# Optimization experiments

Measured on AMD Instinct MI355X. Metric: run time of the kernel, lower is better.

Reference implementation:

```python
import jax, jax.numpy as jnp
import numpy as np

NUM_BUOYS = 16384
TIME_STEPS = 8
FEATURE_DIM = 64
ID_EMB_DIM = 1024  # must equal gru_hidden_size for steps 4/5 to type-check
HIDDEN = 1024
NUM_EMB = 100
INPUT_SIZE = FEATURE_DIM + ID_EMB_DIM


def setup_inputs() -> dict:
    key = jax.random.key(0)
    k = jax.random.split(key, 7)
    s = 1.0 / np.sqrt(HIDDEN)
    return {
        "buoy_obs": jax.random.normal(k[0], (NUM_BUOYS, TIME_STEPS, FEATURE_DIM), jnp.float32),
        "buoy_ids": jax.random.randint(k[1], (NUM_BUOYS,), 0, NUM_EMB),
        "emb": jax.random.normal(k[2], (NUM_EMB, ID_EMB_DIM), jnp.float32),
        "W_ih": jax.random.uniform(k[3], (3 * HIDDEN, INPUT_SIZE), jnp.float32, -s, s),
        "W_hh": jax.random.uniform(k[4], (3 * HIDDEN, HIDDEN), jnp.float32, -s, s),
        "b_ih": jax.random.uniform(k[5], (3 * HIDDEN,), jnp.float32, -s, s),
        "b_hh": jax.random.uniform(k[6], (3 * HIDDEN,), jnp.float32, -s, s),
    }


def _gru_cell(x, h, W_ih, W_hh, b_ih, b_hh):
    # PyTorch GRU gate layout: [r, z, n]
    gi = x @ W_ih.T + b_ih  # (N, 3H)
    gh = h @ W_hh.T + b_hh  # (N, 3H)
    gi_r, gi_z, gi_n = jnp.split(gi, 3, axis=-1)
    gh_r, gh_z, gh_n = jnp.split(gh, 3, axis=-1)
    r = jax.nn.sigmoid(gi_r + gh_r)
    z = jax.nn.sigmoid(gi_z + gh_z)
    n = jnp.tanh(gi_n + r * gh_n)
    return (1.0 - z) * n + z * h


def reference(buoy_obs, buoy_ids, emb, W_ih, W_hh, b_ih, b_hh):
    num_buoys = buoy_obs.shape[0]
    id_emb = emb[buoy_ids]  # (N, E)
    h = jnp.zeros((num_buoys, HIDDEN), buoy_obs.dtype)
    outs = []
    # three unrolled steps: input = [obs_t, id_emb]
    for t in range(3):
        x = jnp.concatenate([buoy_obs[:, t, :], id_emb], axis=-1)
        h = _gru_cell(x, h, W_ih, W_hh, b_ih, b_hh)
        outs.append(h)
    # step 4: input = [out0, obs_1]
    x = jnp.concatenate([outs[0], buoy_obs[:, 1, :]], axis=-1)
    h = _gru_cell(x, h, W_ih, W_hh, b_ih, b_hh)
    second_out = h
    # step 5: input = [out4, obs_2]
    x = jnp.concatenate([second_out, buoy_obs[:, 2, :]], axis=-1)
    h = _gru_cell(x, h, W_ih, W_hh, b_ih, b_hh)
    # AdaptiveMaxPool1d(1) over a length-1 time axis is identity
    return h[None, :, :]  # (1, N, H)
```

## Files before the change

### kernel.cpp

```cpp
#include <hip/hip_runtime.h>
#include <hip/hip_bf16.h>


typedef __bf16 bf16_8 __attribute__((ext_vector_type(8)));
typedef float  f32_16 __attribute__((ext_vector_type(16)));

#define NBUOY 16384
#define HID   1024
#define BUFSZ 28672

__device__ __forceinline__ void async16(const void* g, void* l) {
    __builtin_amdgcn_global_load_lds(
        (const __attribute__((address_space(1))) unsigned int*)g,
        (__attribute__((address_space(3))) unsigned int*)l, 16, 0, 0);
}
__device__ __forceinline__ float sigm(float x)  { return 1.f / (1.f + __expf(-x)); }
__device__ __forceinline__ float tanh_f(float x){ return 1.f - 2.f / (1.f + __expf(2.f * x)); }

template<int QN, int K>
__device__ __forceinline__ void phase_tiled(
    const __bf16* __restrict__ Ap, long aGS, int aG0,
    const __bf16* __restrict__ Wp, long wGS, int nG0,
    __bf16* ls, f32_16 acc[4][2], int tid, int& buf)
{
    const int lane = tid & 63, wid = tid >> 6;
    const int wm = wid >> 1, wn = wid & 1;
    constexpr int NT = K / 64;

    auto stage = [&](int b, int t) {
        __bf16* dst = ls + b * BUFSZ;
        #pragma unroll
        for (int i = 0; i < 7; ++i) {
            const int blk = wid * 7 + i;
            const __bf16* src;
            if (blk < 32) {
                const int g = blk >> 2, kc = blk & 3;
                src = Ap + (long)(aG0 + g) * aGS + (t * 4 + kc) * 512 + lane * 8;
            } else {
                const int u = blk - 32;
                const int gate = u >> 3, ng = (u >> 2) & 1, kc = u & 3;
                src = Wp + (long)(gate * 32 + nG0 + ng) * wGS + (t * 4 + kc) * 512 + lane * 8;
            }
            async16(src, dst + blk * 512);
        }
    };

    stage(buf, 0);
    #pragma unroll 1
    for (int t = 0; t < NT; ++t) {
        __syncthreads();
        if (t + 1 < NT) stage(buf ^ 1, t + 1);
        const __bf16* base = ls + buf * BUFSZ;
        #pragma unroll
        for (int ks = 0; ks < 4; ++ks) {
            const bf16_8 a0 = *(const bf16_8*)(base + ((wm * 2 + 0) * 4 + ks) * 512 + lane * 8);
            const bf16_8 a1 = *(const bf16_8*)(base + ((wm * 2 + 1) * 4 + ks) * 512 + lane * 8);
            const bf16_8 br = *(const bf16_8*)(base + (32 + ((0 * 2 + wn) * 4 + ks)) * 512 + lane * 8);
            const bf16_8 bz = *(const bf16_8*)(base + (32 + ((1 * 2 + wn) * 4 + ks)) * 512 + lane * 8);
            const bf16_8 bn = *(const bf16_8*)(base + (32 + ((2 * 2 + wn) * 4 + ks)) * 512 + lane * 8);
            acc[0][0]  = __builtin_amdgcn_mfma_f32_32x32x16_bf16(a0, br, acc[0][0], 0, 0, 0);
            acc[0][1]  = __builtin_amdgcn_mfma_f32_32x32x16_bf16(a1, br, acc[0][1], 0, 0, 0);
            acc[1][0]  = __builtin_amdgcn_mfma_f32_32x32x16_bf16(a0, bz, acc[1][0], 0, 0, 0);
            acc[1][1]  = __builtin_amdgcn_mfma_f32_32x32x16_bf16(a1, bz, acc[1][1], 0, 0, 0);
            acc[QN][0] = __builtin_amdgcn_mfma_f32_32x32x16_bf16(a0, bn, acc[QN][0], 0, 0, 0);
            acc[QN][1] = __builtin_amdgcn_mfma_f32_32x32x16_bf16(a1, bn, acc[QN][1], 0, 0, 0);
        }
        buf ^= 1;
    }
}

template<int KIH, int KHH, bool USE_E, bool OUT_F32>
__global__ __launch_bounds__(512, 2)
void gru_step(const __bf16* __restrict__ Aih, long aGS,
              const __bf16* __restrict__ Wih,
              const __bf16* __restrict__ Ahh,
              const __bf16* __restrict__ Whh,
              const float*  __restrict__ E,
              const int*    __restrict__ ids,
              const float*  __restrict__ bih,
              const float*  __restrict__ bhh,
              const __bf16* __restrict__ hprev,
              void* __restrict__ outp, long sOut)
{
    __shared__ __bf16 ls[2 * BUFSZ];
    const int tid  = threadIdx.x;
    const int lane = tid & 63, wid = tid >> 6;
    const int wm = wid >> 1, wn = wid & 1;
    const int l31 = lane & 31, hi = lane >> 5;
    const int bid = blockIdx.x;
    const int c = bid & 7, s = bid >> 3;
    const int xb = (c >> 1) * 4 + (s & 3);
    const int yb = (c & 1) * 32 + (s >> 2);
    const int m0 = yb * 256;
    const int n0 = xb * 64;

    f32_16 acc[4][2];
    #pragma unroll
    for (int q = 0; q < 4; ++q)
        #pragma unroll
        for (int mt = 0; mt < 2; ++mt) acc[q][mt] = (f32_16)(0.0f);

    int buf = 0;
    phase_tiled<2, KIH>(Aih, aGS, m0 >> 5, Wih, 34816, n0 >> 5, ls, acc, tid, buf);
    if (KHH > 0)
        phase_tiled<3, KHH>(Ahh, 34816, m0 >> 5, Whh, 32768, n0 >> 5, ls, acc, tid, buf);

    const int col = n0 + wn * 32 + l31;
    const float bhr = bhh[col], bhz = bhh[1024 + col], bhn = bhh[2048 + col];
    float cir = 0.f, ciz = 0.f, cin = 0.f;
    if (!USE_E) { cir = bih[col]; ciz = bih[1024 + col]; cin = bih[2048 + col]; }
    const long colPk = (long)(col >> 4) * 512 + ((col >> 3) & 1) * 256 + (col & 7);

    #pragma unroll
    for (int mt = 0; mt < 2; ++mt) {
        const int g = (m0 >> 5) + wm * 2 + mt;
        #pragma unroll
        for (int reg = 0; reg < 16; ++reg) {
            const int r = 4 * hi + (reg & 3) + 8 * (reg >> 2);
            const int row = g * 32 + r;
            float er = cir, ez = ciz, en = cin;
            if (USE_E) {
                const float* Ep = E + (long)ids[row] * 3072 + col;
                er = Ep[0]; ez = Ep[1024]; en = Ep[2048];
            }
            const float rr = sigm(acc[0][mt][reg] + er + bhr);
            const float z  = sigm(acc[1][mt][reg] + ez + bhz);
            const float nn = tanh_f(acc[2][mt][reg] + en + rr * (acc[3][mt][reg] + bhn));
            float hp = 0.f;
            if (KHH > 0) hp = (float)hprev[(long)g * 34816 + r * 8 + colPk];
            const float h = (1.f - z) * nn + z * hp;
            if (OUT_F32) ((float*)outp)[(long)row * sOut + col] = h;
            else        ((__bf16*)outp)[(long)g * 34816 + r * 8 + colPk] = (__bf16)h;
        }
    }
}

__global__ void pack_W(const float* __restrict__ W, __bf16* __restrict__ P, int K)
{
    const int q  = blockIdx.x * 256 + threadIdx.x;
    const int kc = q % (K >> 3), row = q / (K >> 3);
    const float4 v0 = *(const float4*)(W + (long)row * K + kc * 8);
    const float4 v1 = *(const float4*)(W + (long)row * K + kc * 8 + 4);
    bf16_8 b;
    b[0] = (__bf16)v0.x; b[1] = (__bf16)v0.y; b[2] = (__bf16)v0.z; b[3] = (__bf16)v0.w;
    b[4] = (__bf16)v1.x; b[5] = (__bf16)v1.y; b[6] = (__bf16)v1.z; b[7] = (__bf16)v1.w;
    const long cidx = (long)(row >> 5) * (K * 4)
                    + (kc >> 1) * 64 + (kc & 1) * 32 + (row & 31);
    ((bf16_8*)P)[cidx] = b;
}

__global__ void build_obs(const float* __restrict__ obs,
                          __bf16* __restrict__ O0, __bf16* __restrict__ O1,
                          __bf16* __restrict__ O2,
                          __bf16* __restrict__ X0, __bf16* __restrict__ X1)
{
    const int q = blockIdx.x * 256 + threadIdx.x;
    const int row = q / 24, c = q % 24;
    const int t = c >> 3, kc = c & 7;
    const float4 v0 = *(const float4*)(obs + (long)row * 512 + t * 64 + kc * 8);
    const float4 v1 = *(const float4*)(obs + (long)row * 512 + t * 64 + kc * 8 + 4);
    bf16_8 b;
    b[0] = (__bf16)v0.x; b[1] = (__bf16)v0.y; b[2] = (__bf16)v0.z; b[3] = (__bf16)v0.w;
    b[4] = (__bf16)v1.x; b[5] = (__bf16)v1.y; b[6] = (__bf16)v1.z; b[7] = (__bf16)v1.w;
    const int g = row >> 5, r = row & 31;
    const long ci = (long)g * 256 + (kc >> 1) * 64 + (kc & 1) * 32 + r;
    __bf16* O = (t == 0) ? O0 : (t == 1) ? O1 : O2;
    ((bf16_8*)O)[ci] = b;
    const long cx = (long)g * 4352 + (64 + (kc >> 1)) * 64 + (kc & 1) * 32 + r;
    if (t == 1) ((bf16_8*)X0)[cx] = b;
    if (t == 2) ((bf16_8*)X1)[cx] = b;
}

#define ETILE 10
__global__ void compute_E(const float* __restrict__ emb, const float* __restrict__ Wih,
                          const float* __restrict__ bih, float* __restrict__ E)
{
    __shared__ float semb[ETILE * 1024];
    const int e0 = blockIdx.x * ETILE;
    const int j  = blockIdx.y * 256 + threadIdx.x;
    for (int i = threadIdx.x; i < ETILE * 1024; i += 256)
        semb[i] = emb[(long)(e0 + (i >> 10)) * 1024 + (i & 1023)];
    __syncthreads();
    const float* wp = Wih + (long)j * 1088 + 64;
    float a[ETILE];
    const float b = bih[j];
    #pragma unroll
    for (int t = 0; t < ETILE; ++t) a[t] = b;
    for (int k = 0; k < 1024; k += 4) {
        const float4 w = *(const float4*)(wp + k);
        #pragma unroll
        for (int t = 0; t < ETILE; ++t) {
            const float* se = semb + t * 1024 + k;
            a[t] += se[0] * w.x + se[1] * w.y + se[2] * w.z + se[3] * w.w;
        }
    }
    #pragma unroll
    for (int t = 0; t < ETILE; ++t) E[(long)(e0 + t) * 3072 + j] = a[t];
}

extern "C" void kernel_launch(void* const* d_in, const int* in_sizes, int n_in,
                              void* d_out, int out_size, void* d_ws, size_t ws_size,
                              hipStream_t stream)
{
    const float* obs = (const float*)d_in[0];
    const int*   ids = (const int*)  d_in[1];
    const float* emb = (const float*)d_in[2];
    const float* Wih = (const float*)d_in[3];
    const float* Whh = (const float*)d_in[4];
    const float* bih = (const float*)d_in[5];
    const float* bhh = (const float*)d_in[6];
    float* out = (float*)d_out;

    const size_t MB = 1 << 20;
    const size_t XB = (size_t)NBUOY * 1088 * 2;
    const size_t NEEDED = 22 * MB + 3 * XB;
    if (ws_size < NEEDED) return;

    char* ws = (char*)d_ws;
    float*  E    = (float*) ws;
    __bf16* PWih = (__bf16*)(ws + 2 * MB);
    __bf16* PWhh = (__bf16*)(ws + 9 * MB);
    __bf16* O0   = (__bf16*)(ws + 16 * MB);
    __bf16* O1   = (__bf16*)(ws + 18 * MB);
    __bf16* O2   = (__bf16*)(ws + 20 * MB);
    __bf16* X0   = (__bf16*)(ws + 22 * MB);
    __bf16* X1   = (__bf16*)(ws + 22 * MB + XB);
    __bf16* X2   = (__bf16*)(ws + 22 * MB + 2 * XB);

    dim3 blk(256);
    dim3 blkG(512);
    dim3 gridG(16 * 64);

    pack_W<<<3072 * 1088 / 8 / 256, blk, 0, stream>>>(Wih, PWih, 1088);
    pack_W<<<3072 * 1024 / 8 / 256, blk, 0, stream>>>(Whh, PWhh, 1024);
    build_obs<<<NBUOY * 24 / 256, blk, 0, stream>>>(obs, O0, O1, O2, X0, X1);
    compute_E<<<dim3(10, 12), blk, 0, stream>>>(emb, Wih, bih, E);

    gru_step<64, 0, true, false><<<gridG, blkG, 0, stream>>>(
        O0, 2048, PWih, nullptr, PWhh, E, ids, bih, bhh, nullptr, X0, 0);
    gru_step<64, 1024, true, false><<<gridG, blkG, 0, stream>>>(
        O1, 2048, PWih, X0, PWhh, E, ids, bih, bhh, X0, X1, 0);
    gru_step<64, 1024, true, false><<<gridG, blkG, 0, stream>>>(
        O2, 2048, PWih, X1, PWhh, E, ids, bih, bhh, X1, X2, 0);
    gru_step<1088, 1024, false, false><<<gridG, blkG, 0, stream>>>(
        X0, 34816, PWih, X2, PWhh, nullptr, ids, bih, bhh, X2, X1, 0);
    gru_step<1088, 1024, false, true><<<gridG, blkG, 0, stream>>>(
        X1, 34816, PWih, X1, PWhh, nullptr, ids, bih, bhh, X1, out, 1024);
}
```

Before: 939.3 us.

## Replace double-buffered K-loop with 4-deep pipelined ring and unified ih/hh phases

Restructures the GEMM main loop from a two-buffer, 64-wide K tile into a four-slot ring of 32-wide K tiles, prefetched two tiles ahead. Each wave waits with a counted vmcnt instead of a full drain, and a raw s_barrier replaces __syncthreads. The input and hidden phases are merged into one continuous loop so the pipeline does not refill between them. Load work is split so waves 0-3 load A and waves 4-7 load W, and MFMA issue is raised with s_setprio. The risks are more barriers per unit of K and fragile hand-written waitcnt correctness, although total LDS use stays the same.

```diff
diff --git a/kernel.cpp b/kernel.cpp
--- a/kernel.cpp
+++ b/kernel.cpp
@@ -7,7 +7,7 @@
 
 #define NBUOY 16384
 #define HID   1024
-#define BUFSZ 28672
+#define TBUF  14336
 
 __device__ __forceinline__ void async16(const void* g, void* l) {
     __builtin_amdgcn_global_load_lds(
@@ -17,56 +17,36 @@
 __device__ __forceinline__ float sigm(float x)  { return 1.f / (1.f + __expf(-x)); }
 __device__ __forceinline__ float tanh_f(float x){ return 1.f - 2.f / (1.f + __expf(2.f * x)); }
 
-template<int QN, int K>
-__device__ __forceinline__ void phase_tiled(
-    const __bf16* __restrict__ Ap, long aGS, int aG0,
-    const __bf16* __restrict__ Wp, long wGS, int nG0,
-    __bf16* ls, f32_16 acc[4][2], int tid, int& buf)
-{
-    const int lane = tid & 63, wid = tid >> 6;
-    const int wm = wid >> 1, wn = wid & 1;
-    constexpr int NT = K / 64;
-
-    auto stage = [&](int b, int t) {
-        __bf16* dst = ls + b * BUFSZ;
-        #pragma unroll
-        for (int i = 0; i < 7; ++i) {
-            const int blk = wid * 7 + i;
-            const __bf16* src;
-            if (blk < 32) {
-                const int g = blk >> 2, kc = blk & 3;
-                src = Ap + (long)(aG0 + g) * aGS + (t * 4 + kc) * 512 + lane * 8;
-            } else {
-                const int u = blk - 32;
-                const int gate = u >> 3, ng = (u >> 2) & 1, kc = u & 3;
-                src = Wp + (long)(gate * 32 + nG0 + ng) * wGS + (t * 4 + kc) * 512 + lane * 8;
-            }
-            async16(src, dst + blk * 512);
-        }
-    };
-
-    stage(buf, 0);
-    #pragma unroll 1
-    for (int t = 0; t < NT; ++t) {
-        __syncthreads();
-        if (t + 1 < NT) stage(buf ^ 1, t + 1);
-        const __bf16* base = ls + buf * BUFSZ;
-        #pragma unroll
-        for (int ks = 0; ks < 4; ++ks) {
-            const bf16_8 a0 = *(const bf16_8*)(base + ((wm * 2 + 0) * 4 + ks) * 512 + lane * 8);
-            const bf16_8 a1 = *(const bf16_8*)(base + ((wm * 2 + 1) * 4 + ks) * 512 + lane * 8);
-            const bf16_8 br = *(const bf16_8*)(base + (32 + ((0 * 2 + wn) * 4 + ks)) * 512 + lane * 8);
-            const bf16_8 bz = *(const bf16_8*)(base + (32 + ((1 * 2 + wn) * 4 + ks)) * 512 + lane * 8);
-            const bf16_8 bn = *(const bf16_8*)(base + (32 + ((2 * 2 + wn) * 4 + ks)) * 512 + lane * 8);
-            acc[0][0]  = __builtin_amdgcn_mfma_f32_32x32x16_bf16(a0, br, acc[0][0], 0, 0, 0);
-            acc[0][1]  = __builtin_amdgcn_mfma_f32_32x32x16_bf16(a1, br, acc[0][1], 0, 0, 0);
-            acc[1][0]  = __builtin_amdgcn_mfma_f32_32x32x16_bf16(a0, bz, acc[1][0], 0, 0, 0);
-            acc[1][1]  = __builtin_amdgcn_mfma_f32_32x32x16_bf16(a1, bz, acc[1][1], 0, 0, 0);
-            acc[QN][0] = __builtin_amdgcn_mfma_f32_32x32x16_bf16(a0, bn, acc[QN][0], 0, 0, 0);
-            acc[QN][1] = __builtin_amdgcn_mfma_f32_32x32x16_bf16(a1, bn, acc[QN][1], 0, 0, 0);
-        }
-        buf ^= 1;
-    }
+#define WAITV(n) asm volatile("s_waitcnt vmcnt(" #n ")" ::: "memory")
+
+template<int QN>
+__device__ __forceinline__ void compute_tile(
+    const __bf16* base, f32_16 acc[4][2], int wm, int wn, int lane)
+{
+    const bf16_8 a00 = *(const bf16_8*)(base + ((wm * 2 + 0) * 2 + 0) * 512 + lane * 8);
+    const bf16_8 a10 = *(const bf16_8*)(base + ((wm * 2 + 1) * 2 + 0) * 512 + lane * 8);
+    const bf16_8 br0 = *(const bf16_8*)(base + (16 + 0 * 4 + wn * 2 + 0) * 512 + lane * 8);
+    const bf16_8 bz0 = *(const bf16_8*)(base + (16 + 1 * 4 + wn * 2 + 0) * 512 + lane * 8);
+    const bf16_8 bn0 = *(const bf16_8*)(base + (16 + 2 * 4 + wn * 2 + 0) * 512 + lane * 8);
+    const bf16_8 a01 = *(const bf16_8*)(base + ((wm * 2 + 0) * 2 + 1) * 512 + lane * 8);
+    const bf16_8 a11 = *(const bf16_8*)(base + ((wm * 2 + 1) * 2 + 1) * 512 + lane * 8);
+    const bf16_8 br1 = *(const bf16_8*)(base + (16 + 0 * 4 + wn * 2 + 1) * 512 + lane * 8);
+    const bf16_8 bz1 = *(const bf16_8*)(base + (16 + 1 * 4 + wn * 2 + 1) * 512 + lane * 8);
+    const bf16_8 bn1 = *(const bf16_8*)(base + (16 + 2 * 4 + wn * 2 + 1) * 512 + lane * 8);
+    __builtin_amdgcn_s_setprio(1);
+    acc[0][0]  = __builtin_amdgcn_mfma_f32_32x32x16_bf16(a00, br0, acc[0][0], 0, 0, 0);
+    acc[0][1]  = __builtin_amdgcn_mfma_f32_32x32x16_bf16(a10, br0, acc[0][1], 0, 0, 0);
+    acc[1][0]  = __builtin_amdgcn_mfma_f32_32x32x16_bf16(a00, bz0, acc[1][0], 0, 0, 0);
+    acc[1][1]  = __builtin_amdgcn_mfma_f32_32x32x16_bf16(a10, bz0, acc[1][1], 0, 0, 0);
+    acc[QN][0] = __builtin_amdgcn_mfma_f32_32x32x16_bf16(a00, bn0, acc[QN][0], 0, 0, 0);
+    acc[QN][1] = __builtin_amdgcn_mfma_f32_32x32x16_bf16(a10, bn0, acc[QN][1], 0, 0, 0);
+    acc[0][0]  = __builtin_amdgcn_mfma_f32_32x32x16_bf16(a01, br1, acc[0][0], 0, 0, 0);
+    acc[0][1]  = __builtin_amdgcn_mfma_f32_32x32x16_bf16(a11, br1, acc[0][1], 0, 0, 0);
+    acc[1][0]  = __builtin_amdgcn_mfma_f32_32x32x16_bf16(a01, bz1, acc[1][0], 0, 0, 0);
+    acc[1][1]  = __builtin_amdgcn_mfma_f32_32x32x16_bf16(a11, bz1, acc[1][1], 0, 0, 0);
+    acc[QN][0] = __builtin_amdgcn_mfma_f32_32x32x16_bf16(a01, bn1, acc[QN][0], 0, 0, 0);
+    acc[QN][1] = __builtin_amdgcn_mfma_f32_32x32x16_bf16(a11, bn1, acc[QN][1], 0, 0, 0);
+    __builtin_amdgcn_s_setprio(0);
 }
 
 template<int KIH, int KHH, bool USE_E, bool OUT_F32>
@@ -82,7 +62,9 @@
               const __bf16* __restrict__ hprev,
               void* __restrict__ outp, long sOut)
 {
-    __shared__ __bf16 ls[2 * BUFSZ];
+    __shared__ __bf16 ls[4 * TBUF];
+    constexpr int NTIH = KIH / 32;
+    constexpr int NT   = NTIH + KHH / 32;
     const int tid  = threadIdx.x;
     const int lane = tid & 63, wid = tid >> 6;
     const int wm = wid >> 1, wn = wid & 1;
@@ -91,8 +73,8 @@
     const int c = bid & 7, s = bid >> 3;
     const int xb = (c >> 1) * 4 + (s & 3);
     const int yb = (c & 1) * 32 + (s >> 2);
-    const int m0 = yb * 256;
-    const int n0 = xb * 64;
+    const int aG0 = yb * 8;
+    const int nG0 = xb * 2;
 
     f32_16 acc[4][2];
     #pragma unroll
@@ -100,12 +82,52 @@
         #pragma unroll
         for (int mt = 0; mt < 2; ++mt) acc[q][mt] = (f32_16)(0.0f);
 
-    int buf = 0;
-    phase_tiled<2, KIH>(Aih, aGS, m0 >> 5, Wih, 34816, n0 >> 5, ls, acc, tid, buf);
-    if (KHH > 0)
-        phase_tiled<3, KHH>(Ahh, 34816, m0 >> 5, Whh, 32768, n0 >> 5, ls, acc, tid, buf);
-
-    const int col = n0 + wn * 32 + l31;
+    auto stage = [&](int tt) {
+        if (tt >= NT) return;
+        __bf16* dst = ls + (tt & 3) * TBUF;
+        const __bf16* Ab; long aS; const __bf16* Wb; long wS; int kc2;
+        if (tt < NTIH) { Ab = Aih; aS = aGS;   Wb = Wih; wS = 34816; kc2 = tt * 2; }
+        else           { Ab = Ahh; aS = 34816; Wb = Whh; wS = 32768; kc2 = (tt - NTIH) * 2; }
+        if (wid < 4) {
+            #pragma unroll
+            for (int i = 0; i < 4; ++i) {
+                const int blk = wid * 4 + i;
+                async16(Ab + (long)(aG0 + (blk >> 1)) * aS + (kc2 + (blk & 1)) * 512 + lane * 8,
+                        dst + blk * 512);
+            }
+        } else {
+            #pragma unroll
+            for (int i = 0; i < 3; ++i) {
+                const int u = (wid - 4) * 3 + i;
+                async16(Wb + (long)((u >> 2) * 32 + nG0 + ((u >> 1) & 1)) * wS
+                           + (kc2 + (u & 1)) * 512 + lane * 8,
+                        dst + (16 + u) * 512);
+            }
+        }
+    };
+
+    stage(0); stage(1);
+    #pragma unroll 1
+    for (int tt = 0; tt < NT - 1; ++tt) {
+        stage(tt + 2);
+        __builtin_amdgcn_sched_barrier(0);
+        if (wid < 4) { WAITV(4); } else { WAITV(3); }
+        __builtin_amdgcn_s_barrier();
+        __builtin_amdgcn_sched_barrier(0);
+        const __bf16* base = ls + (tt & 3) * TBUF;
+        if (tt < NTIH) compute_tile<2>(base, acc, wm, wn, lane);
+        else           compute_tile<3>(base, acc, wm, wn, lane);
+    }
+    WAITV(0);
+    __builtin_amdgcn_s_barrier();
+    __builtin_amdgcn_sched_barrier(0);
+    {
+        const __bf16* base = ls + ((NT - 1) & 3) * TBUF;
+        if (NT - 1 < NTIH) compute_tile<2>(base, acc, wm, wn, lane);
+        else               compute_tile<3>(base, acc, wm, wn, lane);
+    }
+
+    const int col = nG0 * 32 + wn * 32 + l31;
     const float bhr = bhh[col], bhz = bhh[1024 + col], bhn = bhh[2048 + col];
     float cir = 0.f, ciz = 0.f, cin = 0.f;
     if (!USE_E) { cir = bih[col]; ciz = bih[1024 + col]; cin = bih[2048 + col]; }
@@ -113,7 +135,7 @@
 
     #pragma unroll
     for (int mt = 0; mt < 2; ++mt) {
-        const int g = (m0 >> 5) + wm * 2 + mt;
+        const int g = aG0 + wm * 2 + mt;
         #pragma unroll
         for (int reg = 0; reg < 16; ++reg) {
             const int r = 4 * hi + (reg & 3) + 8 * (reg >> 2);
```

After: 2.424 ms. 2.58x slower.

## Load weight fragments directly into registers instead of staging via LDS

Applied to the files above, without the earlier changes.

The GEMM inner loop now stages only the activation tiles through LDS with async global-to-LDS copies. Each wave loads its weight fragments for the three gates straight from global memory into registers every k-tile, so the shared buffer shrinks from 28672 to 16384 bf16 elements per stage. This cuts LDS traffic and footprint, which could allow more occupancy. In exchange the weight loads are synchronous, are not prefetched a tile ahead, and are duplicated across the four waves that share the same wn, so memory latency may be exposed.

```diff
diff --git a/kernel.cpp b/kernel.cpp
--- a/kernel.cpp
+++ b/kernel.cpp
@@ -7,7 +7,7 @@
 
 #define NBUOY 16384
 #define HID   1024
-#define BUFSZ 28672
+#define ABUF  16384
 
 __device__ __forceinline__ void async16(const void* g, void* l) {
     __builtin_amdgcn_global_load_lds(
@@ -18,7 +18,7 @@
 __device__ __forceinline__ float tanh_f(float x){ return 1.f - 2.f / (1.f + __expf(2.f * x)); }
 
 template<int QN, int K>
-__device__ __forceinline__ void phase_tiled(
+__device__ __forceinline__ void phase_hybrid(
     const __bf16* __restrict__ Ap, long aGS, int aG0,
     const __bf16* __restrict__ Wp, long wGS, int nG0,
     __bf16* ls, f32_16 acc[4][2], int tid, int& buf)
@@ -27,43 +27,39 @@
     const int wm = wid >> 1, wn = wid & 1;
     constexpr int NT = K / 64;
 
-    auto stage = [&](int b, int t) {
-        __bf16* dst = ls + b * BUFSZ;
-        #pragma unroll
-        for (int i = 0; i < 7; ++i) {
-            const int blk = wid * 7 + i;
-            const __bf16* src;
-            if (blk < 32) {
-                const int g = blk >> 2, kc = blk & 3;
-                src = Ap + (long)(aG0 + g) * aGS + (t * 4 + kc) * 512 + lane * 8;
-            } else {
-                const int u = blk - 32;
-                const int gate = u >> 3, ng = (u >> 2) & 1, kc = u & 3;
-                src = Wp + (long)(gate * 32 + nG0 + ng) * wGS + (t * 4 + kc) * 512 + lane * 8;
-            }
-            async16(src, dst + blk * 512);
+    auto stageA = [&](int b, int t) {
+        __bf16* dst = ls + b * ABUF;
+        #pragma unroll
+        for (int i = 0; i < 4; ++i) {
+            const int blk = wid * 4 + i;
+            async16(Ap + (long)(aG0 + (blk >> 2)) * aGS + (t * 4 + (blk & 3)) * 512 + lane * 8,
+                    dst + blk * 512);
         }
     };
 
-    stage(buf, 0);
+    stageA(buf, 0);
     #pragma unroll 1
     for (int t = 0; t < NT; ++t) {
         __syncthreads();
-        if (t + 1 < NT) stage(buf ^ 1, t + 1);
-        const __bf16* base = ls + buf * BUFSZ;
+        if (t + 1 < NT) stageA(buf ^ 1, t + 1);
+        bf16_8 B[3][4];
+        #pragma unroll
+        for (int g = 0; g < 3; ++g)
+            #pragma unroll
+            for (int ks = 0; ks < 4; ++ks)
+                B[g][ks] = *(const bf16_8*)(Wp + (long)(g * 32 + nG0 + wn) * wGS
+                                               + (t * 4 + ks) * 512 + lane * 8);
+        const __bf16* base = ls + buf * ABUF;
         #pragma unroll
         for (int ks = 0; ks < 4; ++ks) {
             const bf16_8 a0 = *(const bf16_8*)(base + ((wm * 2 + 0) * 4 + ks) * 512 + lane * 8);
             const bf16_8 a1 = *(const bf16_8*)(base + ((wm * 2 + 1) * 4 + ks) * 512 + lane * 8);
-            const bf16_8 br = *(const bf16_8*)(base + (32 + ((0 * 2 + wn) * 4 + ks)) * 512 + lane * 8);
-            const bf16_8 bz = *(const bf16_8*)(base + (32 + ((1 * 2 + wn) * 4 + ks)) * 512 + lane * 8);
-            const bf16_8 bn = *(const bf16_8*)(base + (32 + ((2 * 2 + wn) * 4 + ks)) * 512 + lane * 8);
-            acc[0][0]  = __builtin_amdgcn_mfma_f32_32x32x16_bf16(a0, br, acc[0][0], 0, 0, 0);
-            acc[0][1]  = __builtin_amdgcn_mfma_f32_32x32x16_bf16(a1, br, acc[0][1], 0, 0, 0);
-            acc[1][0]  = __builtin_amdgcn_mfma_f32_32x32x16_bf16(a0, bz, acc[1][0], 0, 0, 0);
-            acc[1][1]  = __builtin_amdgcn_mfma_f32_32x32x16_bf16(a1, bz, acc[1][1], 0, 0, 0);
-            acc[QN][0] = __builtin_amdgcn_mfma_f32_32x32x16_bf16(a0, bn, acc[QN][0], 0, 0, 0);
-            acc[QN][1] = __builtin_amdgcn_mfma_f32_32x32x16_bf16(a1, bn, acc[QN][1], 0, 0, 0);
+            acc[0][0]  = __builtin_amdgcn_mfma_f32_32x32x16_bf16(a0, B[0][ks], acc[0][0], 0, 0, 0);
+            acc[0][1]  = __builtin_amdgcn_mfma_f32_32x32x16_bf16(a1, B[0][ks], acc[0][1], 0, 0, 0);
+            acc[1][0]  = __builtin_amdgcn_mfma_f32_32x32x16_bf16(a0, B[1][ks], acc[1][0], 0, 0, 0);
+            acc[1][1]  = __builtin_amdgcn_mfma_f32_32x32x16_bf16(a1, B[1][ks], acc[1][1], 0, 0, 0);
+            acc[QN][0] = __builtin_amdgcn_mfma_f32_32x32x16_bf16(a0, B[2][ks], acc[QN][0], 0, 0, 0);
+            acc[QN][1] = __builtin_amdgcn_mfma_f32_32x32x16_bf16(a1, B[2][ks], acc[QN][1], 0, 0, 0);
         }
         buf ^= 1;
     }
@@ -82,7 +78,7 @@
               const __bf16* __restrict__ hprev,
               void* __restrict__ outp, long sOut)
 {
-    __shared__ __bf16 ls[2 * BUFSZ];
+    __shared__ __bf16 ls[2 * ABUF];
     const int tid  = threadIdx.x;
     const int lane = tid & 63, wid = tid >> 6;
     const int wm = wid >> 1, wn = wid & 1;
@@ -91,8 +87,8 @@
     const int c = bid & 7, s = bid >> 3;
     const int xb = (c >> 1) * 4 + (s & 3);
     const int yb = (c & 1) * 32 + (s >> 2);
-    const int m0 = yb * 256;
-    const int n0 = xb * 64;
+    const int aG0 = yb * 8;
+    const int nG0 = xb * 2;
 
     f32_16 acc[4][2];
     #pragma unroll
@@ -101,11 +97,11 @@
         for (int mt = 0; mt < 2; ++mt) acc[q][mt] = (f32_16)(0.0f);
 
     int buf = 0;
-    phase_tiled<2, KIH>(Aih, aGS, m0 >> 5, Wih, 34816, n0 >> 5, ls, acc, tid, buf);
+    phase_hybrid<2, KIH>(Aih, aGS, aG0, Wih, 34816, nG0, ls, acc, tid, buf);
     if (KHH > 0)
-        phase_tiled<3, KHH>(Ahh, 34816, m0 >> 5, Whh, 32768, n0 >> 5, ls, acc, tid, buf);
-
-    const int col = n0 + wn * 32 + l31;
+        phase_hybrid<3, KHH>(Ahh, 34816, aG0, Whh, 32768, nG0, ls, acc, tid, buf);
+
+    const int col = nG0 * 32 + wn * 32 + l31;
     const float bhr = bhh[col], bhz = bhh[1024 + col], bhn = bhh[2048 + col];
     float cir = 0.f, ciz = 0.f, cin = 0.f;
     if (!USE_E) { cir = bih[col]; ciz = bih[1024 + col]; cin = bih[2048 + col]; }
@@ -113,7 +109,7 @@
 
     #pragma unroll
     for (int mt = 0; mt < 2; ++mt) {
-        const int g = (m0 >> 5) + wm * 2 + mt;
+        const int g = aG0 + wm * 2 + mt;
         #pragma unroll
         for (int reg = 0; reg < 16; ++reg) {
             const int r = 4 * hi + (reg & 3) + 8 * (reg >> 2);
```

Measured after the change: 1.490 ms. +58.7%, slower.
